# Optimization experiments

Hardware: AMD Instinct MI355X
Metric: run time of the kernel (lower is better)

## Reference

```python
import jax, jax.numpy as jnp
import numpy as np

N, D = 16384, 256

def setup_inputs() -> dict:
    key = jax.random.key(0)
    k1, k2 = jax.random.split(key)
    image_emb = jax.random.normal(k1, (N, D), dtype=jnp.float32)
    text_emb = jax.random.normal(k2, (N, D), dtype=jnp.float32)
    return {"image_emb": image_emb, "text_emb": text_emb}

def reference(image_emb, text_emb):
    n = image_emb.shape[0]
    # [n, n] similarity logits
    logits = image_emb @ text_emb.T
    labels = jnp.arange(n)
    # cross-entropy with diagonal labels: -log_softmax(logits)[i, i]
    logp_t = jax.nn.log_softmax(logits, axis=-1)        # image -> text (rows)
    logp_i = jax.nn.log_softmax(logits.T, axis=-1)      # text -> image (cols)
    loss_t = -logp_t[labels, labels]
    loss_i = -logp_i[labels, labels]
    loss = ((loss_i + loss_t) * 0.5).mean()
    return loss
```

## Files before the change

kernel.cpp:

```cpp
#include <hip/hip_runtime.h>
#include <hip/hip_bf16.h>

#define NN 16384
#define DD 256

typedef unsigned short u16;
typedef unsigned int u32;
typedef unsigned char u8;
typedef long i64;
typedef __attribute__((ext_vector_type(4))) float f32x4;
typedef __attribute__((ext_vector_type(4))) int i32x4;
typedef __attribute__((ext_vector_type(8))) int i32x8;

__global__ __launch_bounds__(256) void prep_kernel(
        const float* __restrict__ img, const float* __restrict__ txt,
        u8* __restrict__ A8, u8* __restrict__ B8,
        float* __restrict__ zbuf ,
        float* __restrict__ out) {
    __shared__ u32 sA[16 * 65 + 8];
    __shared__ u32 sB[16 * 65 + 8];
    const int t = threadIdx.x, bi = blockIdx.x;
    const float4* ib = (const float4*)img + ((size_t)bi << 10);
    const float4* tb = (const float4*)txt + ((size_t)bi << 10);
    const float S = 1.44269504088896f;
    #pragma unroll
    for (int k = 0; k < 4; ++k) {
        const int idx = (k << 8) + t;
        const int row = idx >> 6, col = idx & 63;
        float4 va = ib[idx];
        int pa = __builtin_amdgcn_cvt_pk_fp8_f32(va.x * S, va.y * S, 0, false);
        pa     = __builtin_amdgcn_cvt_pk_fp8_f32(va.z * S, va.w * S, pa, true);
        sA[row * 65 + col] = (u32)pa;
        float4 vb = tb[idx];
        int pb = __builtin_amdgcn_cvt_pk_fp8_f32(vb.x, vb.y, 0, false);
        pb     = __builtin_amdgcn_cvt_pk_fp8_f32(vb.z, vb.w, pb, true);
        sB[row * 65 + col] = (u32)pb;
    }
    __syncthreads();
    const int w = t >> 6, l = t & 63;
    const int k2 = w >> 1, jj = w & 1, qq = l >> 4, mm = l & 15;
    const int wb = mm * 65 + (k2 << 5) + (qq << 3) + (jj << 2);
    i32x4 oa = { (int)sA[wb], (int)sA[wb + 1], (int)sA[wb + 2], (int)sA[wb + 3] };
    i32x4 ob = { (int)sB[wb], (int)sB[wb + 1], (int)sB[wb + 2], (int)sB[wb + 3] };
    const size_t dst = ((size_t)(bi >> 3) << 15) + (k2 << 14) + ((size_t)(bi & 7) << 11)
                     + (jj << 10) + (qq << 8) + (mm << 4);
    *(i32x4*)(A8 + dst) = oa;
    *(i32x4*)(B8 + dst) = ob;
    const int gid = (bi << 8) + t;
    if (gid < 32768) zbuf[gid] = 0.0f;
    if (gid == 0) out[0] = 0.0f;
}

__global__ __launch_bounds__(256, 2) void gemm_lse_kernel(
        const u8* __restrict__ A8, const u8* __restrict__ B8,
        float* __restrict__ s_row, float* __restrict__ s_col,
        float* __restrict__ diag) {
    const int t = threadIdx.x;
    const int lane = t & 63;
    const int w = t >> 6;
    const int wr = w >> 1, wc = w & 1;
    const int q = lane >> 4, m = lane & 15;
    const int bi = blockIdx.x & 127;
    const int jg = blockIdx.x >> 7;
    const int row0 = bi << 7;

    const u8* Aw = A8 + ((size_t)bi << 15) + ((size_t)lane << 4);
    i32x8 areg[2][4];
    #pragma unroll
    for (int k2 = 0; k2 < 2; ++k2)
        #pragma unroll
        for (int rb = 0; rb < 4; ++rb) {
            const u8* p = Aw + (k2 << 14) + (((wr << 2) + rb) << 11);
            i32x4 lo = *(const i32x4*)(p);
            i32x4 hi = *(const i32x4*)(p + 1024);
            areg[k2][rb] = __builtin_shufflevector(lo, hi, 0, 1, 2, 3, 4, 5, 6, 7);
        }

    const f32x4 fzero = {0.f, 0.f, 0.f, 0.f};
    f32x4 accA[4][2], accB[4][2];
    f32x4 rp[4] = {fzero, fzero, fzero, fzero};
    float cpartT = 0.0f;

    const u8* Bw = B8 + (wc << 13) + ((size_t)lane << 4);

    i32x8 bf0, bf1, bf2, bf3;

    auto load_slot = [&](i32x8& bank, int jt_, int ii) {
        const int ct = (jg << 4) | ((jt_ + bi) & 15);
        const u8* pp = Bw + ((size_t)ct << 15) + ((ii >> 2) << 12)
                     + (((ii >> 1) & 1) << 14) + ((ii & 1) << 11);
        i32x4 lo = *(const i32x4*)(pp);
        i32x4 hi = *(const i32x4*)(pp + 1024);
        bank = __builtin_shufflevector(lo, hi, 0, 1, 2, 3, 4, 5, 6, 7);
    };

    auto mfma_slot = [&](f32x4 (&acc)[4][2], const i32x8& bank, int k2_, int cbl_) {
        const f32x4 cinit = {-144.f, -144.f, -144.f, -144.f};
        if (k2_ == 0) {
            #pragma unroll
            for (int rb = 0; rb < 4; ++rb)
                acc[rb][cbl_] = __builtin_amdgcn_mfma_scale_f32_16x16x128_f8f6f4(
                    areg[0][rb], bank, cinit, 0, 0, 0, 127, 0, 127);
        } else {
            #pragma unroll
            for (int rb = 0; rb < 4; ++rb)
                acc[rb][cbl_] = __builtin_amdgcn_mfma_scale_f32_16x16x128_f8f6f4(
                    areg[1][rb], bank, acc[rb][cbl_], 0, 0, 0, 127, 0, 127);
        }
    };

    auto epilogue_half = [&](f32x4 (&acc)[4][2], int jt_, int h) {
        const int ct = (jg << 4) | ((jt_ + bi) & 15);
        if (bi == ct && wr == wc) {
            #pragma unroll
            for (int rb = 0; rb < 4; ++rb)
                if ((rb >> 1) == h) {
                    #pragma unroll
                    for (int r = 0; r < 4; ++r)
                        if (m == ((q << 2) | r))
                            diag[row0 + (wr << 6) + (rb << 4) + m] = acc[rb][rb & 1][r];
                }
        }
        #pragma unroll
        for (int rb = 0; rb < 4; ++rb)
            #pragma unroll
            for (int cb = 0; cb < 2; ++cb)
                #pragma unroll
                for (int r = 0; r < 4; ++r)
                    acc[rb][cb][r] = __builtin_amdgcn_exp2f(acc[rb][cb][r]);
        #pragma unroll
        for (int rb = 0; rb < 4; ++rb)
            rp[rb] += acc[rb][0] + acc[rb][1];
        #pragma unroll
        for (int cb = 0; cb < 2; ++cb) {
            f32x4 s = (acc[0][cb] + acc[1][cb]) + (acc[2][cb] + acc[3][cb]);
            float v = (s[0] + s[1]) + (s[2] + s[3]);
            v += __shfl_xor(v, 16, 64);
            v += __shfl_xor(v, 32, 64);
            if (q == ((h << 1) | cb)) cpartT = v;
        }
        if (h == 1) {
            const int col0 = ct << 7;
            atomicAdd(&s_col[col0 + (wc << 6) + (q << 4) + m], cpartT);
        }
    };

    load_slot(bf0, 0, 0);
    load_slot(bf1, 0, 1);
    #pragma unroll 1
    for (int jt = 0; jt < 16; ++jt) {
        load_slot(bf2, jt, 2);  mfma_slot(accA, bf0, 0, 0);
        load_slot(bf3, jt, 3);  mfma_slot(accA, bf1, 0, 1);
        load_slot(bf0, jt, 4);  mfma_slot(accA, bf2, 1, 0);
        load_slot(bf1, jt, 5);  mfma_slot(accA, bf3, 1, 1);
        if (jt > 0) epilogue_half(accB, jt - 1, 1);
        load_slot(bf2, jt, 6);  mfma_slot(accB, bf0, 0, 0);
        load_slot(bf3, jt, 7);  mfma_slot(accB, bf1, 0, 1);
        if (jt < 15) load_slot(bf0, jt + 1, 0);
        mfma_slot(accB, bf2, 1, 0);
        if (jt < 15) load_slot(bf1, jt + 1, 1);
        mfma_slot(accB, bf3, 1, 1);
        epilogue_half(accA, jt, 0);
    }
    epilogue_half(accB, 15, 1);

    float rout = 0.0f;
    #pragma unroll
    for (int rb = 0; rb < 4; ++rb)
        #pragma unroll
        for (int r = 0; r < 4; ++r) {
            float v = rp[rb][r];
            v += __shfl_xor(v, 1, 16);
            v += __shfl_xor(v, 2, 16);
            v += __shfl_xor(v, 4, 16);
            v += __shfl_xor(v, 8, 16);
            if (m == ((rb << 2) | r)) rout = v;
        }
    atomicAdd(&s_row[row0 + (wr << 6) + ((m >> 2) << 4) + (q << 2) + (m & 3)], rout);
}

__global__ void final_kernel(const float* __restrict__ s_row, const float* __restrict__ s_col,
                             const float* __restrict__ diag, float* __restrict__ out) {
    __shared__ double red[256];
    int t = threadIdx.x;
    int i = blockIdx.x * 256 + t;
    double p = 0.5 * (double)(log2f(s_row[i]) + log2f(s_col[i])) - (double)diag[i];
    red[t] = p;
    __syncthreads();
    for (int s = 128; s > 0; s >>= 1) {
        if (t < s) red[t] += red[t + s];
        __syncthreads();
    }
    if (t == 0) atomicAdd(out, (float)(red[0] * 0.6931471805599453 / (double)NN));
}

extern "C" void kernel_launch(void* const* d_in, const int* in_sizes, int n_in,
                              void* d_out, int out_size, void* d_ws, size_t ws_size,
                              hipStream_t stream) {
    const float* img = (const float*)d_in[0];
    const float* txt = (const float*)d_in[1];
    char* ws = (char*)d_ws;
    u8*    A8    = (u8*)ws;
    u8*    B8    = (u8*)(ws + 4194304);
    float* s_row = (float*)(ws + 8388608);
    float* s_col = (float*)(ws + 8388608 + 65536);
    float* diag  = (float*)(ws + 8388608 + 131072);
    float* out   = (float*)d_out;

    prep_kernel<<<1024, 256, 0, stream>>>(img, txt, A8, B8, s_row, out);
    gemm_lse_kernel<<<1024, 256, 0, stream>>>(A8, B8, s_row, s_col, diag);
    final_kernel<<<64, 256, 0, stream>>>(s_row, s_col, diag, out);
}
```

Baseline: 145.1 us.

## Recompute diagonal in final kernel, peel pipeline loop, add MFMA schedule groups

Drops the diagonal-extraction branch from the GEMM epilogue and instead recomputes each diagonal dot product from the packed fp8 operands in the final reduction kernel, adding back the -144 bias offset. The first and last iterations of the main tile loop are peeled so the steady-state body has no conditional loads or epilogues. sched_group_barrier hints are added to interleave MFMA, VMEM, VALU and transcendental instructions. This trades a little extra work in the small final kernel for a leaner GEMM inner loop, at the risk that the forced schedule raises register pressure or reorders instructions badly.

```diff
diff --git a/kernel.cpp b/kernel.cpp
--- a/kernel.cpp
+++ b/kernel.cpp
@@ -53,8 +53,7 @@
 
 __global__ __launch_bounds__(256, 2) void gemm_lse_kernel(
         const u8* __restrict__ A8, const u8* __restrict__ B8,
-        float* __restrict__ s_row, float* __restrict__ s_col,
-        float* __restrict__ diag) {
+        float* __restrict__ s_row, float* __restrict__ s_col) {
     const int t = threadIdx.x;
     const int lane = t & 63;
     const int w = t >> 6;
@@ -111,16 +110,6 @@
 
     auto epilogue_half = [&](f32x4 (&acc)[4][2], int jt_, int h) {
         const int ct = (jg << 4) | ((jt_ + bi) & 15);
-        if (bi == ct && wr == wc) {
-            #pragma unroll
-            for (int rb = 0; rb < 4; ++rb)
-                if ((rb >> 1) == h) {
-                    #pragma unroll
-                    for (int r = 0; r < 4; ++r)
-                        if (m == ((q << 2) | r))
-                            diag[row0 + (wr << 6) + (rb << 4) + m] = acc[rb][rb & 1][r];
-                }
-        }
         #pragma unroll
         for (int rb = 0; rb < 4; ++rb)
             #pragma unroll
@@ -147,21 +136,47 @@
 
     load_slot(bf0, 0, 0);
     load_slot(bf1, 0, 1);
+    load_slot(bf2, 0, 2);  mfma_slot(accA, bf0, 0, 0);
+    load_slot(bf3, 0, 3);  mfma_slot(accA, bf1, 0, 1);
+    load_slot(bf0, 0, 4);  mfma_slot(accA, bf2, 1, 0);
+    load_slot(bf1, 0, 5);  mfma_slot(accA, bf3, 1, 1);
+    load_slot(bf2, 0, 6);  mfma_slot(accB, bf0, 0, 0);
+    load_slot(bf3, 0, 7);  mfma_slot(accB, bf1, 0, 1);
+    load_slot(bf0, 1, 0);  mfma_slot(accB, bf2, 1, 0);
+    load_slot(bf1, 1, 1);  mfma_slot(accB, bf3, 1, 1);
+    epilogue_half(accA, 0, 0);
+
     #pragma unroll 1
-    for (int jt = 0; jt < 16; ++jt) {
+    for (int jt = 1; jt < 15; ++jt) {
         load_slot(bf2, jt, 2);  mfma_slot(accA, bf0, 0, 0);
         load_slot(bf3, jt, 3);  mfma_slot(accA, bf1, 0, 1);
         load_slot(bf0, jt, 4);  mfma_slot(accA, bf2, 1, 0);
         load_slot(bf1, jt, 5);  mfma_slot(accA, bf3, 1, 1);
-        if (jt > 0) epilogue_half(accB, jt - 1, 1);
+        epilogue_half(accB, jt - 1, 1);
         load_slot(bf2, jt, 6);  mfma_slot(accB, bf0, 0, 0);
         load_slot(bf3, jt, 7);  mfma_slot(accB, bf1, 0, 1);
-        if (jt < 15) load_slot(bf0, jt + 1, 0);
-        mfma_slot(accB, bf2, 1, 0);
-        if (jt < 15) load_slot(bf1, jt + 1, 1);
-        mfma_slot(accB, bf3, 1, 1);
+        load_slot(bf0, jt + 1, 0);  mfma_slot(accB, bf2, 1, 0);
+        load_slot(bf1, jt + 1, 1);  mfma_slot(accB, bf3, 1, 1);
         epilogue_half(accA, jt, 0);
+        #pragma unroll
+        for (int g = 0; g < 16; ++g) {
+            __builtin_amdgcn_sched_group_barrier(0x020, 1, 0);
+            __builtin_amdgcn_sched_group_barrier(0x008, 2, 0);
+            __builtin_amdgcn_sched_group_barrier(0x002, 6, 0);
+            __builtin_amdgcn_sched_group_barrier(0x400, 4, 0);
+        }
     }
+
+    load_slot(bf2, 15, 2);  mfma_slot(accA, bf0, 0, 0);
+    load_slot(bf3, 15, 3);  mfma_slot(accA, bf1, 0, 1);
+    load_slot(bf0, 15, 4);  mfma_slot(accA, bf2, 1, 0);
+    load_slot(bf1, 15, 5);  mfma_slot(accA, bf3, 1, 1);
+    epilogue_half(accB, 14, 1);
+    load_slot(bf2, 15, 6);  mfma_slot(accB, bf0, 0, 0);
+    load_slot(bf3, 15, 7);  mfma_slot(accB, bf1, 0, 1);
+    mfma_slot(accB, bf2, 1, 0);
+    mfma_slot(accB, bf3, 1, 1);
+    epilogue_half(accA, 15, 0);
     epilogue_half(accB, 15, 1);
 
     float rout = 0.0f;
@@ -179,12 +194,38 @@
     atomicAdd(&s_row[row0 + (wr << 6) + ((m >> 2) << 4) + (q << 2) + (m & 3)], rout);
 }
 
-__global__ void final_kernel(const float* __restrict__ s_row, const float* __restrict__ s_col,
-                             const float* __restrict__ diag, float* __restrict__ out) {
+__global__ void final_kernel(const u8* __restrict__ A8, const u8* __restrict__ B8,
+                             const float* __restrict__ s_row, const float* __restrict__ s_col,
+                             float* __restrict__ out) {
     __shared__ double red[256];
     int t = threadIdx.x;
     int i = blockIdx.x * 256 + t;
-    double p = 0.5 * (double)(log2f(s_row[i]) + log2f(s_col[i])) - (double)diag[i];
+    const int pn = i >> 7, r8 = (i >> 4) & 7, mm = i & 15;
+    const u8* pa = A8 + ((size_t)pn << 15) + (r8 << 11) + (mm << 4);
+    const u8* pb = B8 + ((size_t)pn << 15) + (r8 << 11) + (mm << 4);
+    float dot = 0.0f;
+    #pragma unroll
+    for (int k2 = 0; k2 < 2; ++k2)
+        #pragma unroll
+        for (int jj = 0; jj < 2; ++jj)
+            #pragma unroll
+            for (int qq = 0; qq < 4; ++qq) {
+                const int off = (k2 << 14) + (jj << 10) + (qq << 8);
+                i32x4 wa = *(const i32x4*)(pa + off);
+                i32x4 wb = *(const i32x4*)(pb + off);
+                #pragma unroll
+                for (int d = 0; d < 4; ++d) {
+                    dot += __builtin_amdgcn_cvt_f32_fp8(wa[d], 0)
+                         * __builtin_amdgcn_cvt_f32_fp8(wb[d], 0);
+                    dot += __builtin_amdgcn_cvt_f32_fp8(wa[d], 1)
+                         * __builtin_amdgcn_cvt_f32_fp8(wb[d], 1);
+                    dot += __builtin_amdgcn_cvt_f32_fp8(wa[d], 2)
+                         * __builtin_amdgcn_cvt_f32_fp8(wb[d], 2);
+                    dot += __builtin_amdgcn_cvt_f32_fp8(wa[d], 3)
+                         * __builtin_amdgcn_cvt_f32_fp8(wb[d], 3);
+                }
+            }
+    double p = 0.5 * (double)(log2f(s_row[i]) + log2f(s_col[i])) + 144.0 - (double)dot;
     red[t] = p;
     __syncthreads();
     for (int s = 128; s > 0; s >>= 1) {
@@ -204,10 +245,9 @@
     u8*    B8    = (u8*)(ws + 4194304);
     float* s_row = (float*)(ws + 8388608);
     float* s_col = (float*)(ws + 8388608 + 65536);
-    float* diag  = (float*)(ws + 8388608 + 131072);
     float* out   = (float*)d_out;
 
     prep_kernel<<<1024, 256, 0, stream>>>(img, txt, A8, B8, s_row, out);
-    gemm_lse_kernel<<<1024, 256, 0, stream>>>(A8, B8, s_row, s_col, diag);
-    final_kernel<<<64, 256, 0, stream>>>(s_row, s_col, diag, out);
-}
+    gemm_lse_kernel<<<1024, 256, 0, stream>>>(A8, B8, s_row, s_col);
+    final_kernel<<<64, 256, 0, stream>>>(A8, B8, s_row, s_col, out);
+}
```

Result: slower. 161.5 us (+11.3%).
